# Kernel optimization log

Measured on AMD Instinct MI355X. Metric: run time of the kernel, lower is better.

The kernel has to match this reference:

```python
import jax, jax.numpy as jnp
import numpy as np

N_NODES = 100000
N_EDGES = 3200000
F_IN = 512
HIDDEN = 16
N_LABELS = 64


def _degree_norms(edge_src, edge_dst, n):
    # DGL GraphConv norm='both': src side uses out-degree, dst side uses in-degree,
    # both clamped to min 1, raised to -1/2.
    ones = jnp.ones(edge_src.shape[0], dtype=jnp.float32)
    deg_out = jax.ops.segment_sum(ones, edge_src, num_segments=n)
    deg_in = jax.ops.segment_sum(ones, edge_dst, num_segments=n)
    norm_src = jax.lax.rsqrt(jnp.maximum(deg_out, 1.0))
    norm_dst = jax.lax.rsqrt(jnp.maximum(deg_in, 1.0))
    return norm_src, norm_dst


def setup_inputs() -> dict:
    key = jax.random.key(0)
    k_x, k_s, k_d, k_w1, k_b1, k_w2, k_b2 = jax.random.split(key, 7)
    features = jax.random.normal(k_x, (N_NODES, F_IN), dtype=jnp.float32)
    edge_src = jax.random.randint(k_s, (N_EDGES,), 0, N_NODES, dtype=jnp.int64)
    edge_dst = jax.random.randint(k_d, (N_EDGES,), 0, N_NODES, dtype=jnp.int64)
    # GraphConv params (glorot-ish scale)
    W1 = jax.random.normal(k_w1, (F_IN, HIDDEN), dtype=jnp.float32) * (1.0 / np.sqrt(F_IN))
    b1 = jnp.zeros((HIDDEN,), dtype=jnp.float32)
    W2 = jax.random.normal(k_w2, (HIDDEN, N_LABELS), dtype=jnp.float32) * (1.0 / np.sqrt(HIDDEN))
    b2 = jnp.zeros((N_LABELS,), dtype=jnp.float32)
    return {"features": features, "W1": W1, "b1": b1, "W2": W2, "b2": b2,
            "edge_src": edge_src, "edge_dst": edge_dst}


def reference(features, W1, b1, W2, b2, edge_src, edge_dst):
    n = features.shape[0]
    norm_src, norm_dst = _degree_norms(edge_src, edge_dst, n)

    # Layer 1: in_feats (512) > out_feats (16) -> DGL projects first, then aggregates.
    h = features * norm_src[:, None]          # [N, 512]
    h = h @ W1                                 # [N, 16]
    h = jax.ops.segment_sum(h[edge_src], edge_dst, num_segments=n)  # SpMM gather+scatter
    h = h * norm_dst[:, None] + b1
    h = jax.nn.relu(h)  # GraphConv activation; outer F.relu is idempotent

    # Layer 2: in_feats (16) <= out_feats (64) -> DGL aggregates first, then projects.
    h2 = h * norm_src[:, None]                 # [N, 16]
    h2 = jax.ops.segment_sum(h2[edge_src], edge_dst, num_segments=n)
    h2 = h2 * norm_dst[:, None]
    out = h2 @ W2 + b2                          # [N, 64]
    return out
```

## Files before the change

### kernel.cpp

```cpp
#include <hip/hip_runtime.h>

#define N_NODES 100000
#define N_EDGES 3200000
#define F_IN 512
#define HIDDEN 16
#define N_LABELS 64

#define BW 128
#define NBUCK ((N_NODES + BW - 1) / BW)
#define NCB 256
#define SCAN_N (NBUCK * NCB)
#define SCAN_BLKS ((SCAN_N + 1023) / 1024)
#define CAP 10240

__global__ __launch_bounds__(256) void count_kernel(
        const int* __restrict__ es, const int* __restrict__ ed,
        int* __restrict__ Msrc, int* __restrict__ Mdst) {
    __shared__ int h1[NBUCK], h2[NBUCK];
    const int tid = threadIdx.x, g = blockIdx.x;
    for (int i = tid; i < NBUCK; i += 256) { h1[i] = 0; h2[i] = 0; }
    __syncthreads();
    for (int i = g * 256 + tid; i < N_EDGES; i += NCB * 256) {
        atomicAdd(&h1[es[i] >> 7], 1);
        atomicAdd(&h2[ed[i] >> 7], 1);
    }
    __syncthreads();
    for (int i = tid; i < NBUCK; i += 256) {
        Msrc[i * NCB + g] = h1[i];
        Mdst[i * NCB + g] = h2[i];
    }
}

__global__ __launch_bounds__(256) void scanA_kernel(int* __restrict__ a, int* __restrict__ bsum) {
    __shared__ int s[256];
    const int tid = threadIdx.x;
    const int base = blockIdx.x * 1024 + tid * 4;
    int4 v = make_int4(0, 0, 0, 0);
    if (base + 3 < SCAN_N) v = *(const int4*)(a + base);
    else {
        if (base + 0 < SCAN_N) v.x = a[base + 0];
        if (base + 1 < SCAN_N) v.y = a[base + 1];
        if (base + 2 < SCAN_N) v.z = a[base + 2];
        if (base + 3 < SCAN_N) v.w = a[base + 3];
    }
    const int lsum = v.x + v.y + v.z + v.w;
    s[tid] = lsum;
    __syncthreads();
    for (int off = 1; off < 256; off <<= 1) {
        int t = (tid >= off) ? s[tid - off] : 0;
        __syncthreads();
        s[tid] += t;
        __syncthreads();
    }
    int e0 = s[tid] - lsum;
    int e1 = e0 + v.x, e2 = e1 + v.y, e3 = e2 + v.z;
    if (base + 3 < SCAN_N) *(int4*)(a + base) = make_int4(e0, e1, e2, e3);
    else {
        if (base + 0 < SCAN_N) a[base + 0] = e0;
        if (base + 1 < SCAN_N) a[base + 1] = e1;
        if (base + 2 < SCAN_N) a[base + 2] = e2;
        if (base + 3 < SCAN_N) a[base + 3] = e3;
    }
    if (tid == 255) bsum[blockIdx.x] = s[255];
}

__global__ void scanB_kernel(int* __restrict__ bsum) {
    __shared__ int s[256];
    const int tid = threadIdx.x;
    int v = (tid < SCAN_BLKS) ? bsum[tid] : 0;
    s[tid] = v;
    __syncthreads();
    for (int off = 1; off < 256; off <<= 1) {
        int t = (tid >= off) ? s[tid - off] : 0;
        __syncthreads();
        s[tid] += t;
        __syncthreads();
    }
    if (tid < SCAN_BLKS) bsum[tid] = s[tid] - v;
}

__global__ __launch_bounds__(256) void scanC_kernel(int* __restrict__ a, const int* __restrict__ bsum) {
    const int base = blockIdx.x * 1024 + threadIdx.x * 4;
    const int b = bsum[blockIdx.x];
    if (base + 3 < SCAN_N) {
        int4 v = *(int4*)(a + base);
        v.x += b; v.y += b; v.z += b; v.w += b;
        *(int4*)(a + base) = v;
    } else {
        for (int j = 0; j < 4; ++j) if (base + j < SCAN_N) a[base + j] += b;
    }
}

__global__ __launch_bounds__(256) void scatter_kernel(
        const int* __restrict__ es, const int* __restrict__ ed,
        const int* __restrict__ Ssrc, const int* __restrict__ Sdst,
        unsigned* __restrict__ pairs, unsigned char* __restrict__ srcb) {
    __shared__ int c1[NBUCK], c2[NBUCK];
    const int tid = threadIdx.x, g = blockIdx.x;
    for (int i = tid; i < NBUCK; i += 256) {
        c1[i] = Ssrc[i * NCB + g];
        c2[i] = Sdst[i * NCB + g];
    }
    __syncthreads();
    for (int i = g * 256 + tid; i < N_EDGES; i += NCB * 256) {
        int s = es[i], d = ed[i];
        int p2 = atomicAdd(&c2[d >> 7], 1);
        pairs[p2] = ((unsigned)(d & 127) << 17) | (unsigned)s;
        int p1 = atomicAdd(&c1[s >> 7], 1);
        srcb[p1] = (unsigned char)(s & 127);
    }
}

__global__ __launch_bounds__(256) void csr_kernel(
        const int* __restrict__ Sdst, unsigned* __restrict__ pairs,
        int* __restrict__ row_ptr, float* __restrict__ norm_dst) {
    __shared__ unsigned buf[CAP];
    __shared__ int hist[BW], scn[BW], cur[BW];
    const int b = blockIdx.x, tid = threadIdx.x;
    const int base  = Sdst[b * NCB];
    const int nextb = (b == NBUCK - 1) ? N_EDGES : Sdst[(b + 1) * NCB];
    const int nb = nextb - base;
    const bool fits = (nb <= CAP);
    if (tid < BW) hist[tid] = 0;
    __syncthreads();
    for (int i = tid; i < nb; i += 256) {
        unsigned pk = pairs[base + i];
        if (fits) buf[i] = pk;
        atomicAdd(&hist[pk >> 17], 1);
    }
    __syncthreads();
    if (tid < BW) scn[tid] = hist[tid];
    __syncthreads();
    for (int off = 1; off < BW; off <<= 1) {
        int t = 0;
        if (tid < BW && tid >= off) t = scn[tid - off];
        __syncthreads();
        if (tid < BW) scn[tid] += t;
        __syncthreads();
    }
    if (tid < BW) {
        int e = scn[tid] - hist[tid];
        cur[tid] = e;
        int node = b * BW + tid;
        if (node <= N_NODES) row_ptr[node] = base + e;
        if (node < N_NODES) norm_dst[node] = rsqrtf(fmaxf((float)hist[tid], 1.0f));
    }
    __syncthreads();
    if (fits) {
        for (int i = tid; i < nb; i += 256) {
            unsigned pk = buf[i];
            int pos = atomicAdd(&cur[pk >> 17], 1);
            pairs[base + pos] = pk & 0x1FFFFu;
        }
    } else {
        for (int i = tid; i < nb; i += 256)
            pairs[base + i] &= 0x1FFFFu;
    }
}

__global__ __launch_bounds__(256) void srcdeg_kernel(
        const int* __restrict__ Ssrc, const unsigned char* __restrict__ srcb,
        float* __restrict__ norm_src) {
    __shared__ int hist[BW];
    const int b = blockIdx.x, tid = threadIdx.x;
    const int base  = Ssrc[b * NCB];
    const int nextb = (b == NBUCK - 1) ? N_EDGES : Ssrc[(b + 1) * NCB];
    const int nb = nextb - base;
    if (tid < BW) hist[tid] = 0;
    __syncthreads();
    for (int i = tid; i < nb; i += 256)
        atomicAdd(&hist[srcb[base + i]], 1);
    __syncthreads();
    if (tid < BW) {
        int node = b * BW + tid;
        if (node < N_NODES) norm_src[node] = rsqrtf(fmaxf((float)hist[tid], 1.0f));
    }
}

#define MM_NODES 128
#define MM_CH 32
#define MM_S 130
#define KSPLIT 2
#define MM_CHUNKS ((F_IN / MM_CH) / KSPLIT)

__global__ __launch_bounds__(256, 4) void proj1_kernel(
        const float* __restrict__ X, const float* __restrict__ W1,
        float* __restrict__ P0, float* __restrict__ P1) {
    __shared__ float xsT[MM_CH][MM_S];
    __shared__ float w1c[MM_CH][HIDDEN];

    const int tid = threadIdx.x;
    const int node0 = blockIdx.x * MM_NODES;
    const int z = blockIdx.y;
    const int g  = tid >> 2;
    const int kq = (tid & 3) * 4;
    const int c0 = z * MM_CHUNKS;

    float acc[2][4];
#pragma unroll
    for (int a = 0; a < 2; ++a)
#pragma unroll
        for (int b = 0; b < 4; ++b) acc[a][b] = 0.f;

    for (int cc = 0; cc < MM_CHUNKS; ++cc) {
        const int c = c0 + cc;
        __syncthreads();
        if (tid < MM_CH * HIDDEN / 4)
            ((float4*)&w1c[0][0])[tid] = ((const float4*)(W1 + c * MM_CH * HIDDEN))[tid];
#pragma unroll
        for (int it = 0; it < 4; ++it) {
            int i  = tid + it * 256;
            int r  = i >> 3;
            int c4 = i & 7;
            float4 v = make_float4(0.f, 0.f, 0.f, 0.f);
            int gn = node0 + r;
            if (gn < N_NODES)
                v = *((const float4*)(X + (size_t)gn * F_IN + c * MM_CH + c4 * 4));
            int j = c4 * 4;
            xsT[j + 0][r] = v.x;
            xsT[j + 1][r] = v.y;
            xsT[j + 2][r] = v.z;
            xsT[j + 3][r] = v.w;
        }
        __syncthreads();
#pragma unroll
        for (int j = 0; j < MM_CH; ++j) {
            float2 f = *((const float2*)&xsT[j][g * 2]);
            float4 w = *((const float4*)&w1c[j][kq]);
            acc[0][0] += f.x * w.x; acc[0][1] += f.x * w.y; acc[0][2] += f.x * w.z; acc[0][3] += f.x * w.w;
            acc[1][0] += f.y * w.x; acc[1][1] += f.y * w.y; acc[1][2] += f.y * w.z; acc[1][3] += f.y * w.w;
        }
    }

    float* Pz = z ? P1 : P0;
#pragma unroll
    for (int a = 0; a < 2; ++a) {
        int gn = node0 + g * 2 + a;
        if (gn < N_NODES)
            *((float4*)(Pz + (size_t)gn * HIDDEN + kq)) =
                make_float4(acc[a][0], acc[a][1], acc[a][2], acc[a][3]);
    }
}

__global__ void reduce1_kernel(const float* __restrict__ P0, const float* __restrict__ P1,
                               const float* __restrict__ norm_src, float* __restrict__ H1) {
    int gid = blockIdx.x * blockDim.x + threadIdx.x;
    if (gid < N_NODES * 4) {
        float4 a = ((const float4*)P0)[gid];
        float4 b = ((const float4*)P1)[gid];
        float ns = norm_src[gid >> 2];
        ((float4*)H1)[gid] = make_float4((a.x + b.x) * ns, (a.y + b.y) * ns,
                                         (a.z + b.z) * ns, (a.w + b.w) * ns);
    }
}

__global__ __launch_bounds__(256) void spmm1_kernel(
        const int* __restrict__ rp, const int* __restrict__ col,
        const float* __restrict__ H1, const float* __restrict__ norm_dst,
        const float* __restrict__ norm_src, const float* __restrict__ b1,
        float* __restrict__ H1b) {
    int tid = threadIdx.x;
    int node = blockIdx.x * 16 + (tid >> 4);
    int k = tid & 15;
    if (node >= N_NODES) return;
    int beg = rp[node], end = rp[node + 1];
    float acc = 0.f;
    int j = beg;
    for (; j + 3 < end; j += 4) {
        int s0 = col[j], s1 = col[j + 1], s2 = col[j + 2], s3 = col[j + 3];
        float v0 = H1[(size_t)s0 * HIDDEN + k];
        float v1 = H1[(size_t)s1 * HIDDEN + k];
        float v2 = H1[(size_t)s2 * HIDDEN + k];
        float v3 = H1[(size_t)s3 * HIDDEN + k];
        acc += v0 + v1 + v2 + v3;
    }
    for (; j < end; ++j) acc += H1[(size_t)col[j] * HIDDEN + k];
    float v = fmaxf(acc * norm_dst[node] + b1[k], 0.f) * norm_src[node];
    H1b[(size_t)node * HIDDEN + k] = v;
}

__global__ __launch_bounds__(256) void spmm2_final_kernel(
        const int* __restrict__ rp, const int* __restrict__ col,
        const float* __restrict__ H1b, const float* __restrict__ norm_dst,
        const float* __restrict__ W2, const float* __restrict__ b2,
        float* __restrict__ out) {
    __shared__ float w2s[HIDDEN * N_LABELS];
    int tid = threadIdx.x;
    ((float4*)w2s)[tid] = ((const float4*)W2)[tid];
    __syncthreads();

    int node = blockIdx.x * 16 + (tid >> 4);
    int k = tid & 15;
    if (node >= N_NODES) return;
    int beg = rp[node], end = rp[node + 1];
    float acc = 0.f;
    int j = beg;
    for (; j + 3 < end; j += 4) {
        int s0 = col[j], s1 = col[j + 1], s2 = col[j + 2], s3 = col[j + 3];
        float v0 = H1b[(size_t)s0 * HIDDEN + k];
        float v1 = H1b[(size_t)s1 * HIDDEN + k];
        float v2 = H1b[(size_t)s2 * HIDDEN + k];
        float v3 = H1b[(size_t)s3 * HIDDEN + k];
        acc += v0 + v1 + v2 + v3;
    }
    for (; j < end; ++j) acc += H1b[(size_t)col[j] * HIDDEN + k];
    acc *= norm_dst[node];

    float4 o = ((const float4*)b2)[k];
#pragma unroll
    for (int jj = 0; jj < HIDDEN; ++jj) {
        float hj = __shfl(acc, jj, 16);
        float4 w = *((const float4*)&w2s[jj * N_LABELS + 4 * k]);
        o.x += hj * w.x; o.y += hj * w.y; o.z += hj * w.z; o.w += hj * w.w;
    }
    ((float4*)out)[(size_t)node * 16 + k] = o;
}

extern "C" void kernel_launch(void* const* d_in, const int* in_sizes, int n_in,
                              void* d_out, int out_size, void* d_ws, size_t ws_size,
                              hipStream_t stream) {
    const float* X  = (const float*)d_in[0];
    const float* W1 = (const float*)d_in[1];
    const float* b1 = (const float*)d_in[2];
    const float* W2 = (const float*)d_in[3];
    const float* b2 = (const float*)d_in[4];
    const int* es   = (const int*)d_in[5];
    const int* ed   = (const int*)d_in[6];
    float* out = (float*)d_out;

    char* ws = (char*)d_ws;
    float* norm_src = (float*)ws;  ws += (size_t)N_NODES * 4;
    float* norm_dst = (float*)ws;  ws += (size_t)N_NODES * 4;
    int*   row_ptr  = (int*)ws;    ws += 400016;
    char*  R1 = ws;                ws += (size_t)N_NODES * HIDDEN * 4;
    char*  R2 = ws;                ws += (size_t)N_NODES * HIDDEN * 4;
    char*  R3 = ws;

    unsigned char* srcb = (unsigned char*)R1;
    float* P0  = (float*)R1;
    float* H1  = (float*)R1;
    int*   Sdst = (int*)R2;
    int*   Ssrc = (int*)(R2 + 800768);
    int*   bs1  = (int*)(R2 + 1601536);
    int*   bs2  = (int*)(R2 + 1602560);
    float* P1   = (float*)R2;
    float* H1b  = (float*)R2;
    unsigned* pairs = (unsigned*)R3;
    int*   col  = (int*)R3;

    const int NPB = (N_NODES + MM_NODES - 1) / MM_NODES;

    count_kernel<<<NCB, 256, 0, stream>>>(es, ed, Ssrc, Sdst);
    scanA_kernel<<<SCAN_BLKS, 256, 0, stream>>>(Sdst, bs1);
    scanA_kernel<<<SCAN_BLKS, 256, 0, stream>>>(Ssrc, bs2);
    scanB_kernel<<<1, 256, 0, stream>>>(bs1);
    scanB_kernel<<<1, 256, 0, stream>>>(bs2);
    scanC_kernel<<<SCAN_BLKS, 256, 0, stream>>>(Sdst, bs1);
    scanC_kernel<<<SCAN_BLKS, 256, 0, stream>>>(Ssrc, bs2);
    scatter_kernel<<<NCB, 256, 0, stream>>>(es, ed, Ssrc, Sdst, pairs, srcb);
    csr_kernel<<<NBUCK, 256, 0, stream>>>(Sdst, pairs, row_ptr, norm_dst);
    srcdeg_kernel<<<NBUCK, 256, 0, stream>>>(Ssrc, srcb, norm_src);
    proj1_kernel<<<dim3(NPB, KSPLIT), 256, 0, stream>>>(X, W1, P0, P1);
    reduce1_kernel<<<(N_NODES * 4 + 255) / 256, 256, 0, stream>>>(P0, P1, norm_src, H1);
    spmm1_kernel<<<(N_NODES + 15) / 16, 256, 0, stream>>>(row_ptr, col, H1, norm_dst, norm_src, b1, H1b);
    spmm2_final_kernel<<<(N_NODES + 15) / 16, 256, 0, stream>>>(row_ptr, col, H1b, norm_dst, W2, b2, out);
}
```

Before: 598.1 us.

## Double-buffer proj1 with async LDS loads, fuse reduction, batch scan launches

Rewrites the layer-1 projection to stream X into double-buffered, XOR-swizzled LDS through global_load_lds, overlapping the next chunk's load with compute. It drops the K-split and the separate reduce kernel, applying norm_src in the epilogue, and reads W1 straight from global memory. The paired scan kernels are merged into single launches using blockIdx.y, and count/scatter move to 512-thread blocks. The aim is to cut kernel launches and the partial-sum traffic, and to hide X load latency, at the cost of fewer blocks for the projection.

```diff
diff --git a/kernel.cpp b/kernel.cpp
--- a/kernel.cpp
+++ b/kernel.cpp
@@ -13,25 +13,29 @@
 #define SCAN_BLKS ((SCAN_N + 1023) / 1024)
 #define CAP 10240
 
-__global__ __launch_bounds__(256) void count_kernel(
+__global__ __launch_bounds__(512) void count_kernel(
         const int* __restrict__ es, const int* __restrict__ ed,
         int* __restrict__ Msrc, int* __restrict__ Mdst) {
     __shared__ int h1[NBUCK], h2[NBUCK];
     const int tid = threadIdx.x, g = blockIdx.x;
-    for (int i = tid; i < NBUCK; i += 256) { h1[i] = 0; h2[i] = 0; }
-    __syncthreads();
-    for (int i = g * 256 + tid; i < N_EDGES; i += NCB * 256) {
+    for (int i = tid; i < NBUCK; i += 512) { h1[i] = 0; h2[i] = 0; }
+    __syncthreads();
+    for (int i = g * 512 + tid; i < N_EDGES; i += NCB * 512) {
         atomicAdd(&h1[es[i] >> 7], 1);
         atomicAdd(&h2[ed[i] >> 7], 1);
     }
     __syncthreads();
-    for (int i = tid; i < NBUCK; i += 256) {
+    for (int i = tid; i < NBUCK; i += 512) {
         Msrc[i * NCB + g] = h1[i];
         Mdst[i * NCB + g] = h2[i];
     }
 }
 
-__global__ __launch_bounds__(256) void scanA_kernel(int* __restrict__ a, int* __restrict__ bsum) {
+__global__ __launch_bounds__(256) void scanA_kernel(
+        int* __restrict__ a0, int* __restrict__ a1,
+        int* __restrict__ b0, int* __restrict__ b1) {
+    int* a    = blockIdx.y ? a1 : a0;
+    int* bsum = blockIdx.y ? b1 : b0;
     __shared__ int s[256];
     const int tid = threadIdx.x;
     const int base = blockIdx.x * 1024 + tid * 4;
@@ -64,7 +68,8 @@
     if (tid == 255) bsum[blockIdx.x] = s[255];
 }
 
-__global__ void scanB_kernel(int* __restrict__ bsum) {
+__global__ void scanB_kernel(int* __restrict__ b0, int* __restrict__ b1) {
+    int* bsum = blockIdx.y ? b1 : b0;
     __shared__ int s[256];
     const int tid = threadIdx.x;
     int v = (tid < SCAN_BLKS) ? bsum[tid] : 0;
@@ -79,7 +84,11 @@
     if (tid < SCAN_BLKS) bsum[tid] = s[tid] - v;
 }
 
-__global__ __launch_bounds__(256) void scanC_kernel(int* __restrict__ a, const int* __restrict__ bsum) {
+__global__ __launch_bounds__(256) void scanC_kernel(
+        int* __restrict__ a0, int* __restrict__ a1,
+        const int* __restrict__ b0, const int* __restrict__ b1) {
+    int* a = blockIdx.y ? a1 : a0;
+    const int* bsum = blockIdx.y ? b1 : b0;
     const int base = blockIdx.x * 1024 + threadIdx.x * 4;
     const int b = bsum[blockIdx.x];
     if (base + 3 < SCAN_N) {
@@ -91,18 +100,18 @@
     }
 }
 
-__global__ __launch_bounds__(256) void scatter_kernel(
+__global__ __launch_bounds__(512) void scatter_kernel(
         const int* __restrict__ es, const int* __restrict__ ed,
         const int* __restrict__ Ssrc, const int* __restrict__ Sdst,
         unsigned* __restrict__ pairs, unsigned char* __restrict__ srcb) {
     __shared__ int c1[NBUCK], c2[NBUCK];
     const int tid = threadIdx.x, g = blockIdx.x;
-    for (int i = tid; i < NBUCK; i += 256) {
+    for (int i = tid; i < NBUCK; i += 512) {
         c1[i] = Ssrc[i * NCB + g];
         c2[i] = Sdst[i * NCB + g];
     }
     __syncthreads();
-    for (int i = g * 256 + tid; i < N_EDGES; i += NCB * 256) {
+    for (int i = g * 512 + tid; i < N_EDGES; i += NCB * 512) {
         int s = es[i], d = ed[i];
         int p2 = atomicAdd(&c2[d >> 7], 1);
         pairs[p2] = ((unsigned)(d & 127) << 17) | (unsigned)s;
@@ -177,81 +186,112 @@
     }
 }
 
-#define MM_NODES 128
-#define MM_CH 32
-#define MM_S 130
-#define KSPLIT 2
-#define MM_CHUNKS ((F_IN / MM_CH) / KSPLIT)
-
-__global__ __launch_bounds__(256, 4) void proj1_kernel(
+#define P1_ROWS 256
+#define P1_CH 32
+#define P1_CHUNKS (F_IN / P1_CH)
+#define P1_BLKS ((N_NODES + P1_ROWS - 1) / P1_ROWS)
+
+#define GLD16(gp, lp) __builtin_amdgcn_global_load_lds( \
+    (const __attribute__((address_space(1))) unsigned int*)(gp), \
+    (__attribute__((address_space(3))) unsigned int*)(lp), 16, 0, 0)
+
+__device__ __forceinline__ void p1_stage(const float* __restrict__ X,
+                                         int node0, int c, float* lbuf,
+                                         int srow0, int scg, int wbase) {
+#pragma unroll
+    for (int it = 0; it < 4; ++it) {
+        int row = srow0 + it * 64;
+        int grow = node0 + row;
+        if (grow > N_NODES - 1) grow = N_NODES - 1;
+        int cg = scg ^ ((row >> 2) & 7);
+        const float* gp = X + (size_t)grow * F_IN + (size_t)c * P1_CH + cg * 4;
+        float* lp = lbuf + (size_t)(it * 512 + wbase) * 4;
+        GLD16(gp, lp);
+    }
+}
+
+__global__ __launch_bounds__(512, 4) void proj1_kernel(
         const float* __restrict__ X, const float* __restrict__ W1,
-        float* __restrict__ P0, float* __restrict__ P1) {
-    __shared__ float xsT[MM_CH][MM_S];
-    __shared__ float w1c[MM_CH][HIDDEN];
+        const float* __restrict__ norm_src, float* __restrict__ H1) {
+    __shared__ float xs[2][P1_ROWS * P1_CH];
 
     const int tid = threadIdx.x;
-    const int node0 = blockIdx.x * MM_NODES;
-    const int z = blockIdx.y;
-    const int g  = tid >> 2;
+    const int node0 = blockIdx.x * P1_ROWS;
+
+    const int srow0 = tid >> 3;
+    const int scg   = tid & 7;
+    const int wbase = tid & 448;
+
+    p1_stage(X, node0, 0, &xs[0][0], srow0, scg, wbase);
+    __syncthreads();
+
+    const int rg = tid >> 2;
     const int kq = (tid & 3) * 4;
-    const int c0 = z * MM_CHUNKS;
-
-    float acc[2][4];
+    const int sw = (rg >> 1) & 7;
+
+    float acc0[2][4];
 #pragma unroll
     for (int a = 0; a < 2; ++a)
 #pragma unroll
-        for (int b = 0; b < 4; ++b) acc[a][b] = 0.f;
-
-    for (int cc = 0; cc < MM_CHUNKS; ++cc) {
-        const int c = c0 + cc;
-        __syncthreads();
-        if (tid < MM_CH * HIDDEN / 4)
-            ((float4*)&w1c[0][0])[tid] = ((const float4*)(W1 + c * MM_CH * HIDDEN))[tid];
-#pragma unroll
-        for (int it = 0; it < 4; ++it) {
-            int i  = tid + it * 256;
-            int r  = i >> 3;
-            int c4 = i & 7;
-            float4 v = make_float4(0.f, 0.f, 0.f, 0.f);
-            int gn = node0 + r;
-            if (gn < N_NODES)
-                v = *((const float4*)(X + (size_t)gn * F_IN + c * MM_CH + c4 * 4));
-            int j = c4 * 4;
-            xsT[j + 0][r] = v.x;
-            xsT[j + 1][r] = v.y;
-            xsT[j + 2][r] = v.z;
-            xsT[j + 3][r] = v.w;
+        for (int b = 0; b < 4; ++b) acc0[a][b] = 0.f;
+
+#define P1_COMPUTE(ACC, CC) do {                                              \
+    const float* xb = &xs[(CC) & 1][0];                                       \
+    _Pragma("unroll")                                                         \
+    for (int kk4 = 0; kk4 < 8; ++kk4) {                                       \
+        const int k = (CC) * P1_CH + kk4 * 4;                                 \
+        float4 w0 = *((const float4*)(W1 + (size_t)(k + 0) * HIDDEN + kq));   \
+        float4 w1 = *((const float4*)(W1 + (size_t)(k + 1) * HIDDEN + kq));   \
+        float4 w2 = *((const float4*)(W1 + (size_t)(k + 2) * HIDDEN + kq));   \
+        float4 w3 = *((const float4*)(W1 + (size_t)(k + 3) * HIDDEN + kq));   \
+        _Pragma("unroll")                                                     \
+        for (int a = 0; a < 2; ++a) {                                         \
+            int row = rg * 2 + a;                                             \
+            float4 xv = *((const float4*)&xb[row * P1_CH + ((kk4 ^ sw) * 4)]);\
+            ACC[a][0] += xv.x * w0.x; ACC[a][1] += xv.x * w0.y;               \
+            ACC[a][2] += xv.x * w0.z; ACC[a][3] += xv.x * w0.w;               \
+            ACC[a][0] += xv.y * w1.x; ACC[a][1] += xv.y * w1.y;               \
+            ACC[a][2] += xv.y * w1.z; ACC[a][3] += xv.y * w1.w;               \
+            ACC[a][0] += xv.z * w2.x; ACC[a][1] += xv.z * w2.y;               \
+            ACC[a][2] += xv.z * w2.z; ACC[a][3] += xv.z * w2.w;               \
+            ACC[a][0] += xv.w * w3.x; ACC[a][1] += xv.w * w3.y;               \
+            ACC[a][2] += xv.w * w3.z; ACC[a][3] += xv.w * w3.w;               \
+        }                                                                     \
+    }                                                                         \
+} while (0)
+
+    for (int cc = 0; cc < 8; ++cc) {
+        p1_stage(X, node0, cc + 1, &xs[(cc & 1) ^ 1][0], srow0, scg, wbase);
+        P1_COMPUTE(acc0, cc);
+        __syncthreads();
+    }
+
+    float acc1[2][4];
+#pragma unroll
+    for (int a = 0; a < 2; ++a)
+#pragma unroll
+        for (int b = 0; b < 4; ++b) acc1[a][b] = 0.f;
+
+    for (int cc = 8; cc < P1_CHUNKS; ++cc) {
+        if (cc + 1 < P1_CHUNKS)
+            p1_stage(X, node0, cc + 1, &xs[(cc & 1) ^ 1][0], srow0, scg, wbase);
+        P1_COMPUTE(acc1, cc);
+        __syncthreads();
+    }
+
+#pragma unroll
+    for (int a = 0; a < 2; ++a) {
+        int gn = node0 + rg * 2 + a;
+        if (gn < N_NODES) {
+            float ns = norm_src[gn];
+            *((float4*)(H1 + (size_t)gn * HIDDEN + kq)) =
+                make_float4((acc0[a][0] + acc1[a][0]) * ns,
+                            (acc0[a][1] + acc1[a][1]) * ns,
+                            (acc0[a][2] + acc1[a][2]) * ns,
+                            (acc0[a][3] + acc1[a][3]) * ns);
         }
-        __syncthreads();
-#pragma unroll
-        for (int j = 0; j < MM_CH; ++j) {
-            float2 f = *((const float2*)&xsT[j][g * 2]);
-            float4 w = *((const float4*)&w1c[j][kq]);
-            acc[0][0] += f.x * w.x; acc[0][1] += f.x * w.y; acc[0][2] += f.x * w.z; acc[0][3] += f.x * w.w;
-            acc[1][0] += f.y * w.x; acc[1][1] += f.y * w.y; acc[1][2] += f.y * w.z; acc[1][3] += f.y * w.w;
-        }
-    }
-
-    float* Pz = z ? P1 : P0;
-#pragma unroll
-    for (int a = 0; a < 2; ++a) {
-        int gn = node0 + g * 2 + a;
-        if (gn < N_NODES)
-            *((float4*)(Pz + (size_t)gn * HIDDEN + kq)) =
-                make_float4(acc[a][0], acc[a][1], acc[a][2], acc[a][3]);
-    }
-}
-
-__global__ void reduce1_kernel(const float* __restrict__ P0, const float* __restrict__ P1,
-                               const float* __restrict__ norm_src, float* __restrict__ H1) {
-    int gid = blockIdx.x * blockDim.x + threadIdx.x;
-    if (gid < N_NODES * 4) {
-        float4 a = ((const float4*)P0)[gid];
-        float4 b = ((const float4*)P1)[gid];
-        float ns = norm_src[gid >> 2];
-        ((float4*)H1)[gid] = make_float4((a.x + b.x) * ns, (a.y + b.y) * ns,
-                                         (a.z + b.z) * ns, (a.w + b.w) * ns);
-    }
+    }
+#undef P1_COMPUTE
 }
 
 __global__ __launch_bounds__(256) void spmm1_kernel(
@@ -337,31 +377,23 @@
     char*  R3 = ws;
 
     unsigned char* srcb = (unsigned char*)R1;
-    float* P0  = (float*)R1;
     float* H1  = (float*)R1;
     int*   Sdst = (int*)R2;
     int*   Ssrc = (int*)(R2 + 800768);
     int*   bs1  = (int*)(R2 + 1601536);
     int*   bs2  = (int*)(R2 + 1602560);
-    float* P1   = (float*)R2;
     float* H1b  = (float*)R2;
     unsigned* pairs = (unsigned*)R3;
     int*   col  = (int*)R3;
 
-    const int NPB = (N_NODES + MM_NODES - 1) / MM_NODES;
-
-    count_kernel<<<NCB, 256, 0, stream>>>(es, ed, Ssrc, Sdst);
-    scanA_kernel<<<SCAN_BLKS, 256, 0, stream>>>(Sdst, bs1);
-    scanA_kernel<<<SCAN_BLKS, 256, 0, stream>>>(Ssrc, bs2);
-    scanB_kernel<<<1, 256, 0, stream>>>(bs1);
-    scanB_kernel<<<1, 256, 0, stream>>>(bs2);
-    scanC_kernel<<<SCAN_BLKS, 256, 0, stream>>>(Sdst, bs1);
-    scanC_kernel<<<SCAN_BLKS, 256, 0, stream>>>(Ssrc, bs2);
-    scatter_kernel<<<NCB, 256, 0, stream>>>(es, ed, Ssrc, Sdst, pairs, srcb);
+    count_kernel<<<NCB, 512, 0, stream>>>(es, ed, Ssrc, Sdst);
+    scanA_kernel<<<dim3(SCAN_BLKS, 2), 256, 0, stream>>>(Sdst, Ssrc, bs1, bs2);
+    scanB_kernel<<<dim3(1, 2), 256, 0, stream>>>(bs1, bs2);
+    scanC_kernel<<<dim3(SCAN_BLKS, 2), 256, 0, stream>>>(Sdst, Ssrc, bs1, bs2);
+    scatter_kernel<<<NCB, 512, 0, stream>>>(es, ed, Ssrc, Sdst, pairs, srcb);
     csr_kernel<<<NBUCK, 256, 0, stream>>>(Sdst, pairs, row_ptr, norm_dst);
     srcdeg_kernel<<<NBUCK, 256, 0, stream>>>(Ssrc, srcb, norm_src);
-    proj1_kernel<<<dim3(NPB, KSPLIT), 256, 0, stream>>>(X, W1, P0, P1);
-    reduce1_kernel<<<(N_NODES * 4 + 255) / 256, 256, 0, stream>>>(P0, P1, norm_src, H1);
+    proj1_kernel<<<P1_BLKS, 512, 0, stream>>>(X, W1, norm_src, H1);
     spmm1_kernel<<<(N_NODES + 15) / 16, 256, 0, stream>>>(row_ptr, col, H1, norm_dst, norm_src, b1, H1b);
     spmm2_final_kernel<<<(N_NODES + 15) / 16, 256, 0, stream>>>(row_ptr, col, H1b, norm_dst, W2, b2, out);
 }
```

After: 623.3 us. 1.04x slower.
